# Performance work log

Hardware: AMD Instinct MI355X
Metric: run time of the kernel (lower is better)

## Reference

```python
import jax, jax.numpy as jnp
import numpy as np

B, N, S, K, D = 4, 8192, 2048, 32, 64
RADIUS = 0.2
MLP = [64, 64, 128]
C_IN = 3 + D  # 67
EPS = 1e-5  # BatchNorm eps


def setup_inputs() -> dict:
    key = jax.random.key(0)
    ks = jax.random.split(key, 8)
    inp = {
        "xyz": jax.random.uniform(ks[0], (B, N, 3), dtype=jnp.float32),
        "points": jax.random.normal(ks[1], (B, N, D), dtype=jnp.float32) * 0.1,
    }
    c = C_IN
    for i, o in enumerate(MLP):
        inp[f"w{i}"] = jax.random.normal(ks[2 + i], (o, c), dtype=jnp.float32) / np.sqrt(c).astype(np.float32)
        inp[f"b{i}"] = jnp.zeros((o,), jnp.float32)
        inp[f"g{i}"] = jnp.ones((o,), jnp.float32)
        inp[f"be{i}"] = jnp.zeros((o,), jnp.float32)
        c = o
    return inp


def _farthest_point_sample(xyz, npoint):
    # xyz: [B,N,3] -> idx [B,npoint]. Deterministic start at index 0
    # (torch version uses a random start index).
    Bb, Nn, _ = xyz.shape

    def step(carry, _):
        dist, far = carry
        centroid = jnp.take_along_axis(xyz, far[:, None, None], axis=1)  # [B,1,3]
        d = jnp.sum((xyz - centroid) ** 2, axis=-1)  # [B,N]
        dist = jnp.minimum(dist, d)
        nxt = jnp.argmax(dist, axis=-1).astype(jnp.int32)
        return (dist, nxt), far

    init = (jnp.full((Bb, Nn), 1e18, xyz.dtype), jnp.zeros((Bb,), jnp.int32))
    _, idx = jax.lax.scan(step, init, None, length=npoint)  # [npoint,B]
    return idx.T


def _square_distance(src, dst):
    # src [B,S,3], dst [B,N,3] -> [B,S,N]
    d = -2.0 * jnp.einsum("bsc,bnc->bsn", src, dst)
    d = d + jnp.sum(src ** 2, -1)[:, :, None] + jnp.sum(dst ** 2, -1)[:, None, :]
    return jnp.maximum(d, 0.0)


def _query_ball_point(radius, nsample, xyz, new_xyz):
    Bb, Nn, _ = xyz.shape
    sqr = _square_distance(new_xyz, xyz)  # [B,S,N]
    gi = jnp.broadcast_to(jnp.arange(Nn, dtype=jnp.int32), sqr.shape)
    gi = jnp.where(sqr > radius ** 2, Nn, gi)
    gi = jnp.sort(gi, axis=-1)[..., :nsample]  # [B,S,nsample]
    first = gi[..., :1]
    gi = jnp.where(gi >= Nn, first, gi)
    return jnp.clip(gi, 0, Nn - 1)


def _forward(xyz, points, params):
    bidx = jnp.arange(B)[:, None]
    fps_idx = _farthest_point_sample(xyz, S)          # [B,S]
    new_xyz = xyz[bidx, fps_idx]                      # [B,S,3]
    idx = _query_ball_point(RADIUS, K, xyz, new_xyz)  # [B,S,K]
    bidx3 = jnp.arange(B)[:, None, None]
    grouped_xyz = xyz[bidx3, idx]                     # [B,S,K,3]
    gnorm = grouped_xyz - new_xyz[:, :, None, :]
    gpts = points[bidx3, idx]                         # [B,S,K,D]
    feat = jnp.concatenate([gnorm, gpts], axis=-1)    # [B,S,K,3+D]
    x = jnp.transpose(feat, (0, 3, 2, 1))             # [B,C,K,S]
    for (w, b, g, be) in params:
        x = jnp.einsum("oc,bcks->boks", w, x) + b[None, :, None, None]
        mu = jnp.mean(x, axis=(0, 2, 3), keepdims=True)     # BN training mode
        var = jnp.var(x, axis=(0, 2, 3), keepdims=True)
        x = g[None, :, None, None] * (x - mu) * jax.lax.rsqrt(var + EPS) + be[None, :, None, None]
        x = jax.nn.relu(x)
    new_points = jnp.max(x, axis=2)                   # [B,mlp[-1],S]
    return new_xyz, new_points


def reference(xyz, points, w0, b0, g0, be0, w1, b1, g1, be1, w2, b2, g2, be2):
    params = ((w0, b0, g0, be0), (w1, b1, g1, be1), (w2, b2, g2, be2))
    return _forward(xyz, points, params)
```

## Files before the change

### kernel.cpp

```cpp
#include <hip/hip_runtime.h>
#include <hip/hip_bf16.h>

#define BB 4
#define NN 8192
#define SS 2048
#define KK 32
#define DD 64
#define CIN 67
#define PPIX (BB*SS*KK)
#define CNT_F 262144.0f
#define R2 0.04f
#define BN_EPS 1e-5f

typedef unsigned long long ull;

__global__ void zero_kernel(float* __restrict__ p, int n) {
    int i = blockIdx.x * 256 + threadIdx.x;
    if (i < n) p[i] = 0.0f;
}

__global__ __launch_bounds__(512, 2) void fps_kernel(const float* __restrict__ xyz,
                                                     float* __restrict__ out_newxyz) {
    const int b = blockIdx.x;
    const int t = threadIdx.x;
    const int w = t >> 6, lane = t & 63;
    const float* X = xyz + (size_t)b * NN * 3;

#define FPS_DECL(J) float px##J, py##J, pz##J, ds##J;
    FPS_DECL(0) FPS_DECL(1) FPS_DECL(2) FPS_DECL(3)
    FPS_DECL(4) FPS_DECL(5) FPS_DECL(6) FPS_DECL(7)
    FPS_DECL(8) FPS_DECL(9) FPS_DECL(10) FPS_DECL(11)
    FPS_DECL(12) FPS_DECL(13) FPS_DECL(14) FPS_DECL(15)

#define FPS_LOAD(J) { const int i = t * 16 + J; \
    px##J = X[3*i]; py##J = X[3*i+1]; pz##J = X[3*i+2]; ds##J = 1e18f; }
    FPS_LOAD(0) FPS_LOAD(1) FPS_LOAD(2) FPS_LOAD(3)
    FPS_LOAD(4) FPS_LOAD(5) FPS_LOAD(6) FPS_LOAD(7)
    FPS_LOAD(8) FPS_LOAD(9) FPS_LOAD(10) FPS_LOAD(11)
    FPS_LOAD(12) FPS_LOAD(13) FPS_LOAD(14) FPS_LOAD(15)

    __shared__ ull sKey[2][8];
    __shared__ float sCx[2][8], sCy[2][8], sCz[2][8];

    float cx = X[0], cy = X[1], cz = X[2];

    for (int s = 0; s < SS; s++) {
        if (t == 0) {
            float* o = out_newxyz + (size_t)(b * SS + s) * 3;
            o[0] = cx; o[1] = cy; o[2] = cz;
        }
        float bd = 0.0f;
#define FPS_UPD(J) { \
    float dx = __fsub_rn(px##J, cx); \
    float dy = __fsub_rn(py##J, cy); \
    float dz = __fsub_rn(pz##J, cz); \
    float dd = __fadd_rn(__fadd_rn(__fmul_rn(dx, dx), __fmul_rn(dy, dy)), \
                         __fmul_rn(dz, dz)); \
    ds##J = fminf(ds##J, dd); \
    bd = fmaxf(bd, ds##J); }
        FPS_UPD(0) FPS_UPD(1) FPS_UPD(2) FPS_UPD(3)
        FPS_UPD(4) FPS_UPD(5) FPS_UPD(6) FPS_UPD(7)
        FPS_UPD(8) FPS_UPD(9) FPS_UPD(10) FPS_UPD(11)
        FPS_UPD(12) FPS_UPD(13) FPS_UPD(14) FPS_UPD(15)

        float wm = bd;
#pragma unroll
        for (int off = 32; off; off >>= 1)
            wm = fmaxf(wm, __shfl_xor(wm, off, 64));
        ull eq = __ballot(bd == wm);
        if (lane == __ffsll(eq) - 1) {
            int bj = 0;
            float wx = px0, wy = py0, wz = pz0;
#define FPS_PICK(J) if (ds##J == bd) { bj = J; wx = px##J; wy = py##J; wz = pz##J; }
            FPS_PICK(15) FPS_PICK(14) FPS_PICK(13) FPS_PICK(12)
            FPS_PICK(11) FPS_PICK(10) FPS_PICK(9) FPS_PICK(8)
            FPS_PICK(7) FPS_PICK(6) FPS_PICK(5) FPS_PICK(4)
            FPS_PICK(3) FPS_PICK(2) FPS_PICK(1) FPS_PICK(0)
            sKey[s & 1][w] = ((ull)__float_as_uint(bd) << 32)
                           | (unsigned)(NN - 1 - (t * 16 + bj));
            sCx[s & 1][w] = wx; sCy[s & 1][w] = wy; sCz[s & 1][w] = wz;
        }
        __syncthreads();
        const int par = s & 1;
        ull m = sKey[par][0]; int im = 0;
#pragma unroll
        for (int i = 1; i < 8; i++) {
            ull v = sKey[par][i];
            if (v > m) { m = v; im = i; }
        }
        cx = sCx[par][im]; cy = sCy[par][im]; cz = sCz[par][im];
    }
}

__global__ __launch_bounds__(256) void ball_kernel(const float* __restrict__ xyz,
                                                   const float* __restrict__ newxyz,
                                                   int* __restrict__ idx_out) {
    const int wave = threadIdx.x >> 6;
    const int lane = threadIdx.x & 63;
    const int q = blockIdx.x * 4 + wave;
    const int b = q >> 11;
    const float* X = xyz + (size_t)b * NN * 3;

    float sx = newxyz[(size_t)q * 3 + 0];
    float sy = newxyz[(size_t)q * 3 + 1];
    float sz = newxyz[(size_t)q * 3 + 2];
    float ssum = __fadd_rn(__fadd_rn(__fmul_rn(sx, sx), __fmul_rn(sy, sy)),
                           __fmul_rn(sz, sz));

    __shared__ int sIdx[4][32];
    int* my = sIdx[wave];

    int have = 0;
    for (int base = 0; base < NN && have < KK; base += 64) {
        int i = base + lane;
        float x = X[3 * i], y = X[3 * i + 1], z = X[3 * i + 2];
        float xsum = __fadd_rn(__fadd_rn(__fmul_rn(x, x), __fmul_rn(y, y)),
                               __fmul_rn(z, z));
        float dot = __fadd_rn(__fadd_rn(__fmul_rn(sx, x), __fmul_rn(sy, y)),
                              __fmul_rn(sz, z));
        float d = __fadd_rn(__fadd_rn(__fmul_rn(-2.0f, dot), ssum), xsum);
        d = fmaxf(d, 0.0f);
        bool in = (d <= R2);
        ull mask = __ballot(in);
        int pre = __popcll(mask & ((1ull << lane) - 1ull));
        if (in && (have + pre) < KK) my[have + pre] = i;
        have += __popcll(mask);
    }
    __syncthreads();
    if (lane < KK) {
        int v = (lane < have) ? my[lane] : my[0];
        idx_out[(size_t)q * KK + lane] = v;
    }
}

#define STATS_REDUCE(sumsPtr)                                                      \
    {                                                                              \
        __shared__ float sS[128];                                                  \
        if (threadIdx.x < 128) sS[threadIdx.x] = 0.0f;                             \
        __syncthreads();                                                           \
        _Pragma("unroll") for (int o = 0; o < 64; o++) {                           \
            float s1 = acc[o];                                                     \
            float s2 = __fmul_rn(s1, s1);                                          \
            _Pragma("unroll") for (int off = 32; off; off >>= 1) {                 \
                s1 += __shfl_down(s1, off, 64);                                    \
                s2 += __shfl_down(s2, off, 64);                                    \
            }                                                                      \
            if ((threadIdx.x & 63) == 0) {                                         \
                atomicAdd(&sS[o], s1);                                             \
                atomicAdd(&sS[64 + o], s2);                                        \
            }                                                                      \
        }                                                                          \
        __syncthreads();                                                           \
        if (threadIdx.x < 64)                                                      \
            atomicAdd(&(sumsPtr)[2 * threadIdx.x], sS[threadIdx.x]);               \
        else if (threadIdx.x < 128)                                                \
            atomicAdd(&(sumsPtr)[2 * (threadIdx.x - 64) + 1], sS[threadIdx.x]);    \
    }

#define ACC_C(NOUT4, cc, f)                                                        \
    {                                                                              \
        const float4* wr = (const float4*)(&wT[(cc) * (NOUT4) * 4]);               \
        _Pragma("unroll") for (int o4 = 0; o4 < (NOUT4); o4++) {                   \
            float4 wv = wr[o4];                                                    \
            acc[4 * o4 + 0] = fmaf(wv.x, (f), acc[4 * o4 + 0]);                    \
            acc[4 * o4 + 1] = fmaf(wv.y, (f), acc[4 * o4 + 1]);                    \
            acc[4 * o4 + 2] = fmaf(wv.z, (f), acc[4 * o4 + 2]);                    \
            acc[4 * o4 + 3] = fmaf(wv.w, (f), acc[4 * o4 + 3]);                    \
        }                                                                          \
    }

__global__ __launch_bounds__(256) void layer1_kernel(const float* __restrict__ xyz,
                                                     const float* __restrict__ points,
                                                     const float* __restrict__ newxyz,
                                                     const int* __restrict__ idx,
                                                     const float* __restrict__ w,
                                                     const float* __restrict__ bias,
                                                     float* __restrict__ y,
                                                     float* __restrict__ sums) {
    __shared__ __align__(16) float wT[CIN * 64];
    for (int i = threadIdx.x; i < CIN * 64; i += 256) {
        int o = i / CIN, c = i - o * CIN;
        wT[c * 64 + o] = w[i];
    }
    __syncthreads();

    const int p = blockIdx.x * 256 + threadIdx.x;
    const int b = p >> 16;
    const int sk = p & 65535;
    const int s = sk >> 5;
    const int pt = idx[p];

    const float* xr = xyz + ((size_t)b * NN + pt) * 3;
    const float* nr = newxyz + ((size_t)(b * SS + s)) * 3;
    float g0 = __fsub_rn(xr[0], nr[0]);
    float g1 = __fsub_rn(xr[1], nr[1]);
    float g2 = __fsub_rn(xr[2], nr[2]);

    float acc[64];
#pragma unroll
    for (int o = 0; o < 64; o++) acc[o] = bias[o];

    ACC_C(16, 0, g0);
    ACC_C(16, 1, g1);
    ACC_C(16, 2, g2);

    const float4* prow = (const float4*)(points + ((size_t)b * NN + pt) * DD);
#pragma unroll 4
    for (int c4 = 0; c4 < 16; c4++) {
        float4 f4 = prow[c4];
        ACC_C(16, 3 + 4 * c4 + 0, f4.x);
        ACC_C(16, 3 + 4 * c4 + 1, f4.y);
        ACC_C(16, 3 + 4 * c4 + 2, f4.z);
        ACC_C(16, 3 + 4 * c4 + 3, f4.w);
    }
#pragma unroll 8
    for (int o = 0; o < 64; o++) y[(size_t)o * PPIX + p] = acc[o];

    STATS_REDUCE(sums);
}

__global__ __launch_bounds__(256) void layer_mid_kernel(const float* __restrict__ yin,
                                                        const float* __restrict__ cs,
                                                        const float* __restrict__ csh,
                                                        const float* __restrict__ w,
                                                        const float* __restrict__ bias,
                                                        float* __restrict__ yout,
                                                        float* __restrict__ sums) {
    __shared__ __align__(16) float wT[64 * 64];
    for (int i = threadIdx.x; i < 64 * 64; i += 256) {
        int o = i >> 6, c = i & 63;
        wT[c * 64 + o] = w[i];
    }
    __syncthreads();

    const int p = blockIdx.x * 256 + threadIdx.x;
    float acc[64];
#pragma unroll
    for (int o = 0; o < 64; o++) acc[o] = bias[o];

#pragma unroll 4
    for (int c = 0; c < 64; c++) {
        float f = fmaxf(fmaf(yin[(size_t)c * PPIX + p], cs[c], csh[c]), 0.0f);
        ACC_C(16, c, f);
    }
#pragma unroll 8
    for (int o = 0; o < 64; o++) yout[(size_t)o * PPIX + p] = acc[o];

    STATS_REDUCE(sums);
}

__global__ void coef_kernel(const float* __restrict__ sums,
                            const float* __restrict__ g,
                            const float* __restrict__ be,
                            float* __restrict__ coefOut, int C) {
    int c = threadIdx.x;
    if (c >= C) return;
    float mu = sums[2 * c] * (1.0f / CNT_F);
    float ex2 = sums[2 * c + 1] * (1.0f / CNT_F);
    float var = fmaxf(ex2 - mu * mu, 0.0f);
    float sc = g[c] / sqrtf(var + BN_EPS);
    coefOut[c] = sc;
    coefOut[C + c] = be[c] - mu * sc;
}

__global__ __launch_bounds__(256) void final_kernel(const float* __restrict__ y3,
                                                    const float* __restrict__ coef,
                                                    float* __restrict__ outp) {
    const int gid = blockIdx.x * 256 + threadIdx.x;
    const int s = gid & 2047;
    const int o = (gid >> 11) & 127;
    const int b = gid >> 18;
    const float sc = coef[o], sh = coef[128 + o];
    const float4* row = (const float4*)(y3 + (size_t)o * PPIX + ((size_t)(b * SS + s)) * KK);
    float m = 0.0f;
#pragma unroll
    for (int i = 0; i < 8; i++) {
        float4 v = row[i];
        m = fmaxf(m, fmaf(v.x, sc, sh));
        m = fmaxf(m, fmaf(v.y, sc, sh));
        m = fmaxf(m, fmaf(v.z, sc, sh));
        m = fmaxf(m, fmaf(v.w, sc, sh));
    }
    outp[gid] = m;
}

extern "C" void kernel_launch(void* const* d_in, const int* in_sizes, int n_in,
                              void* d_out, int out_size, void* d_ws, size_t ws_size,
                              hipStream_t stream) {
    const float* xyz = (const float*)d_in[0];
    const float* points = (const float*)d_in[1];
    const float* w0 = (const float*)d_in[2];
    const float* b0 = (const float*)d_in[3];
    const float* g0 = (const float*)d_in[4];
    const float* be0 = (const float*)d_in[5];
    const float* w1 = (const float*)d_in[6];
    const float* b1 = (const float*)d_in[7];
    const float* g1 = (const float*)d_in[8];
    const float* be1 = (const float*)d_in[9];
    const float* w2 = (const float*)d_in[10];
    const float* b2 = (const float*)d_in[11];
    const float* g2 = (const float*)d_in[12];
    const float* be2 = (const float*)d_in[13];
    float* out = (float*)d_out;

    char* ws = (char*)d_ws;
    int* ballIdx = (int*)(ws + (32 << 10));
    float* sums = (float*)(ws + (1 << 20) + (256 << 10));
    float* coef = sums + 768;
    float* y2 = (float*)(ws + (2ull << 20));
    float* y1 = (float*)(ws + (66ull << 20));
    float* y3 = (float*)(ws + (66ull << 20));

    zero_kernel<<<3, 256, 0, stream>>>(sums, 768);

    fps_kernel<<<BB, 512, 0, stream>>>(xyz, out);
    ball_kernel<<<(BB * SS) / 4, 256, 0, stream>>>(xyz, out, ballIdx);

    layer1_kernel<<<PPIX / 256, 256, 0, stream>>>(xyz, points, out, ballIdx, w0, b0,
                                                  y1, sums + 0);
    coef_kernel<<<1, 64, 0, stream>>>(sums + 0, g0, be0, coef + 0, 64);

    layer_mid_kernel<<<PPIX / 256, 256, 0, stream>>>(y1, coef + 0, coef + 64, w1, b1,
                                                     y2, sums + 256);
    coef_kernel<<<1, 64, 0, stream>>>(sums + 256, g1, be1, coef + 256, 64);

    layer_mid_kernel<<<PPIX / 256, 256, 0, stream>>>(y2, coef + 256, coef + 320,
                                                     w2, b2, y3, sums + 512);
    layer_mid_kernel<<<PPIX / 256, 256, 0, stream>>>(y2, coef + 256, coef + 320,
                                                     w2 + 64 * 64, b2 + 64,
                                                     y3 + (size_t)64 * PPIX,
                                                     sums + 512 + 128);
    coef_kernel<<<1, 128, 0, stream>>>(sums + 512, g2, be2, coef + 512, 128);

    final_kernel<<<(BB * 128 * SS) / 256, 256, 0, stream>>>(y3, coef + 512, out + BB * SS * 3);
}
```

Before: 3.508 ms.

## Move BN statistics into separate streaming stats kernel; pin FPS point registers

The per-block shuffle and atomic reduction of BatchNorm sums is taken out of the layer kernels and replaced by a separate stats_kernel that re-reads each layer's output channel-contiguously with float4 loads. This lightens the compute kernels (fewer shuffles, shared atomics and barriers) at the cost of an extra full read of each activation tensor, about 64 to 128 MB per layer. An empty asm barrier is also added in FPS to keep the point coordinates in VGPRs. The summation order for mean and variance changes, which slightly alters floating-point results.

```diff
diff --git a/kernel.cpp b/kernel.cpp
--- a/kernel.cpp
+++ b/kernel.cpp
@@ -38,6 +38,16 @@
     FPS_LOAD(4) FPS_LOAD(5) FPS_LOAD(6) FPS_LOAD(7)
     FPS_LOAD(8) FPS_LOAD(9) FPS_LOAD(10) FPS_LOAD(11)
     FPS_LOAD(12) FPS_LOAD(13) FPS_LOAD(14) FPS_LOAD(15)
+
+#define FPS_OPQ4(A,B,C,D) asm volatile("" : \
+    "+v"(px##A), "+v"(py##A), "+v"(pz##A), \
+    "+v"(px##B), "+v"(py##B), "+v"(pz##B), \
+    "+v"(px##C), "+v"(py##C), "+v"(pz##C), \
+    "+v"(px##D), "+v"(py##D), "+v"(pz##D));
+    FPS_OPQ4(0, 1, 2, 3)
+    FPS_OPQ4(4, 5, 6, 7)
+    FPS_OPQ4(8, 9, 10, 11)
+    FPS_OPQ4(12, 13, 14, 15)
 
     __shared__ ull sKey[2][8];
     __shared__ float sCx[2][8], sCy[2][8], sCz[2][8];
@@ -133,30 +143,6 @@
     }
 }
 
-#define STATS_REDUCE(sumsPtr)                                                      \
-    {                                                                              \
-        __shared__ float sS[128];                                                  \
-        if (threadIdx.x < 128) sS[threadIdx.x] = 0.0f;                             \
-        __syncthreads();                                                           \
-        _Pragma("unroll") for (int o = 0; o < 64; o++) {                           \
-            float s1 = acc[o];                                                     \
-            float s2 = __fmul_rn(s1, s1);                                          \
-            _Pragma("unroll") for (int off = 32; off; off >>= 1) {                 \
-                s1 += __shfl_down(s1, off, 64);                                    \
-                s2 += __shfl_down(s2, off, 64);                                    \
-            }                                                                      \
-            if ((threadIdx.x & 63) == 0) {                                         \
-                atomicAdd(&sS[o], s1);                                             \
-                atomicAdd(&sS[64 + o], s2);                                        \
-            }                                                                      \
-        }                                                                          \
-        __syncthreads();                                                           \
-        if (threadIdx.x < 64)                                                      \
-            atomicAdd(&(sumsPtr)[2 * threadIdx.x], sS[threadIdx.x]);               \
-        else if (threadIdx.x < 128)                                                \
-            atomicAdd(&(sumsPtr)[2 * (threadIdx.x - 64) + 1], sS[threadIdx.x]);    \
-    }
-
 #define ACC_C(NOUT4, cc, f)                                                        \
     {                                                                              \
         const float4* wr = (const float4*)(&wT[(cc) * (NOUT4) * 4]);               \
@@ -175,8 +161,7 @@
                                                      const int* __restrict__ idx,
                                                      const float* __restrict__ w,
                                                      const float* __restrict__ bias,
-                                                     float* __restrict__ y,
-                                                     float* __restrict__ sums) {
+                                                     float* __restrict__ y) {
     __shared__ __align__(16) float wT[CIN * 64];
     for (int i = threadIdx.x; i < CIN * 64; i += 256) {
         int o = i / CIN, c = i - o * CIN;
@@ -215,8 +200,6 @@
     }
 #pragma unroll 8
     for (int o = 0; o < 64; o++) y[(size_t)o * PPIX + p] = acc[o];
-
-    STATS_REDUCE(sums);
 }
 
 __global__ __launch_bounds__(256) void layer_mid_kernel(const float* __restrict__ yin,
@@ -224,8 +207,7 @@
                                                         const float* __restrict__ csh,
                                                         const float* __restrict__ w,
                                                         const float* __restrict__ bias,
-                                                        float* __restrict__ yout,
-                                                        float* __restrict__ sums) {
+                                                        float* __restrict__ yout) {
     __shared__ __align__(16) float wT[64 * 64];
     for (int i = threadIdx.x; i < 64 * 64; i += 256) {
         int o = i >> 6, c = i & 63;
@@ -245,8 +227,36 @@
     }
 #pragma unroll 8
     for (int o = 0; o < 64; o++) yout[(size_t)o * PPIX + p] = acc[o];
-
-    STATS_REDUCE(sums);
+}
+
+__global__ __launch_bounds__(256) void stats_kernel(const float* __restrict__ y,
+                                                    float* __restrict__ sums) {
+    const int c = blockIdx.x >> 5;
+    const int chunk = blockIdx.x & 31;
+    const float4* src = (const float4*)(y + (size_t)c * PPIX + (size_t)chunk * 8192);
+    float s1 = 0.f, s2 = 0.f;
+#pragma unroll
+    for (int it = 0; it < 8; it++) {
+        float4 v = src[(it << 8) + threadIdx.x];
+        s1 += v.x + v.y + v.z + v.w;
+        s2 = fmaf(v.x, v.x, s2);
+        s2 = fmaf(v.y, v.y, s2);
+        s2 = fmaf(v.z, v.z, s2);
+        s2 = fmaf(v.w, v.w, s2);
+    }
+#pragma unroll
+    for (int off = 32; off; off >>= 1) {
+        s1 += __shfl_down(s1, off, 64);
+        s2 += __shfl_down(s2, off, 64);
+    }
+    __shared__ float p1[4], p2[4];
+    int wv = threadIdx.x >> 6;
+    if ((threadIdx.x & 63) == 0) { p1[wv] = s1; p2[wv] = s2; }
+    __syncthreads();
+    if (threadIdx.x == 0) {
+        atomicAdd(&sums[2 * c], p1[0] + p1[1] + p1[2] + p1[3]);
+        atomicAdd(&sums[2 * c + 1], p2[0] + p2[1] + p2[2] + p2[3]);
+    }
 }
 
 __global__ void coef_kernel(const float* __restrict__ sums,
@@ -316,20 +326,20 @@
     fps_kernel<<<BB, 512, 0, stream>>>(xyz, out);
     ball_kernel<<<(BB * SS) / 4, 256, 0, stream>>>(xyz, out, ballIdx);
 
-    layer1_kernel<<<PPIX / 256, 256, 0, stream>>>(xyz, points, out, ballIdx, w0, b0,
-                                                  y1, sums + 0);
+    layer1_kernel<<<PPIX / 256, 256, 0, stream>>>(xyz, points, out, ballIdx, w0, b0, y1);
+    stats_kernel<<<64 * 32, 256, 0, stream>>>(y1, sums + 0);
     coef_kernel<<<1, 64, 0, stream>>>(sums + 0, g0, be0, coef + 0, 64);
 
-    layer_mid_kernel<<<PPIX / 256, 256, 0, stream>>>(y1, coef + 0, coef + 64, w1, b1,
-                                                     y2, sums + 256);
+    layer_mid_kernel<<<PPIX / 256, 256, 0, stream>>>(y1, coef + 0, coef + 64, w1, b1, y2);
+    stats_kernel<<<64 * 32, 256, 0, stream>>>(y2, sums + 256);
     coef_kernel<<<1, 64, 0, stream>>>(sums + 256, g1, be1, coef + 256, 64);
 
     layer_mid_kernel<<<PPIX / 256, 256, 0, stream>>>(y2, coef + 256, coef + 320,
-                                                     w2, b2, y3, sums + 512);
+                                                     w2, b2, y3);
     layer_mid_kernel<<<PPIX / 256, 256, 0, stream>>>(y2, coef + 256, coef + 320,
                                                      w2 + 64 * 64, b2 + 64,
-                                                     y3 + (size_t)64 * PPIX,
-                                                     sums + 512 + 128);
+                                                     y3 + (size_t)64 * PPIX);
+    stats_kernel<<<128 * 32, 256, 0, stream>>>(y3, sums + 512);
     coef_kernel<<<1, 128, 0, stream>>>(sums + 512, g2, be2, coef + 512, 128);
 
     final_kernel<<<(BB * 128 * SS) / 256, 256, 0, stream>>>(y3, coef + 512, out + BB * SS * 3);
```

Result: faster. 3.245 ms (-7.5%).
